# Performance work log

Hardware: AMD Instinct MI355X
Metric: run time of the kernel (lower is better)

The kernel has to match this reference:

```python
import jax, jax.numpy as jnp
import numpy as np

HEADS = 8
DIM_HEAD = 32
SCALE = DIM_HEAD ** -0.5
EPS = 1e-12  # F.normalize eps


def _rmsnorm_ch(t, g):
    # F.normalize(t, dim=1) * g * sqrt(C)  (normalize_dim=1)
    c = t.shape[1]
    norm = jnp.sqrt(jnp.sum(t * t, axis=1, keepdims=True))
    return t / jnp.maximum(norm, EPS) * g[None, :, None, None] * (c ** 0.5)


def setup_inputs() -> dict:
    key = jax.random.key(0)
    ks = jax.random.split(key, 4)
    B, C, H, W = 16, 256, 64, 64
    hidden = HEADS * DIM_HEAD  # 256
    x = jax.random.normal(ks[0], (B, C, H, W), dtype=jnp.float32)
    g1 = jnp.ones((C,), dtype=jnp.float32)
    # conv 1x1 weights stored as [out_ch, in_ch]
    w_qkv = jax.random.normal(ks[1], (hidden * 3, C), dtype=jnp.float32) * (1.0 / np.sqrt(C))
    w_out = jax.random.normal(ks[2], (C, hidden), dtype=jnp.float32) * (1.0 / np.sqrt(hidden))
    b_out = jnp.zeros((C,), dtype=jnp.float32)
    g2 = jnp.ones((C,), dtype=jnp.float32)
    return {"x": x, "g1": g1, "w_qkv": w_qkv, "w_out": w_out, "b_out": b_out, "g2": g2}


def reference(x, g1, w_qkv, w_out, b_out, g2):
    b, c, h, w = x.shape
    n = h * w
    xn = _rmsnorm_ch(x, g1)
    # 1x1 conv (no bias) == channel matmul
    qkv = jnp.einsum('oc,bchw->bohw', w_qkv, xn)
    q, k, v = jnp.split(qkv, 3, axis=1)
    # b (h c) x y -> b h c (x y)
    q = q.reshape(b, HEADS, DIM_HEAD, n)
    k = k.reshape(b, HEADS, DIM_HEAD, n)
    v = v.reshape(b, HEADS, DIM_HEAD, n)
    q = jax.nn.softmax(q, axis=-2) * SCALE  # softmax over dim_head
    k = jax.nn.softmax(k, axis=-1)          # softmax over sequence
    context = jnp.einsum('bhdn,bhen->bhde', k, v)  # [b,h,d,e] small
    out = jnp.einsum('bhde,bhdn->bhen', context, q)
    out = out.reshape(b, HEADS * DIM_HEAD, h, w)
    out = jnp.einsum('oc,bchw->bohw', w_out, out) + b_out[None, :, None, None]
    return _rmsnorm_ch(out, g2) + x
```

## Files before the change

### kernel.cpp

```cpp
#include <hip/hip_runtime.h>
#include <math.h>


#define B_ 16
#define C_ 256
#define N_ 4096
#define SCALE_ 0.17677669529663687f
#define EPS_ 1e-12f

typedef __attribute__((ext_vector_type(8))) short bf16x8;
typedef __attribute__((ext_vector_type(4))) float f32x4;

__device__ __forceinline__ ushort f2bf(float f) {
    union { float f; uint u; } x; x.f = f;
    uint r = (x.u + 0x7FFFu + ((x.u >> 16) & 1u)) >> 16;
    return (ushort)r;
}
__device__ __forceinline__ float bf2f(ushort s) {
    union { uint u; float f; } x; x.u = ((uint)s) << 16;
    return x.f;
}

__global__ __launch_bounds__(256) void k_prep(const float* __restrict__ w_qkv,
                                              const float* __restrict__ g1,
                                              ushort* __restrict__ Wp) {
    int o = blockIdx.x, c = threadIdx.x;
    Wp[(size_t)o * 256 + c] = f2bf(w_qkv[(size_t)o * 256 + c] * g1[c]);
}

__global__ __launch_bounds__(256) void k_xconv(const float* __restrict__ x,
                                               ushort* __restrict__ xnbT) {
    __shared__ float ssp[4][64];
    __shared__ float rinv_s[64];
    __shared__ ushort T[64][268];
    int b = blockIdx.y, n0 = blockIdx.x * 64;
    const float* xb = x + (size_t)b * C_ * N_ + n0;
    int t = threadIdx.x;
    int nl = t & 63, cg = t >> 6;
    float ss = 0.f;
    #pragma unroll 8
    for (int i = 0; i < 64; ++i) {
        float v = xb[(size_t)(cg * 64 + i) * N_ + nl];
        ss += v * v;
    }
    ssp[cg][nl] = ss;
    __syncthreads();
    if (t < 64)
        rinv_s[t] = 16.f / fmaxf(sqrtf(ssp[0][t] + ssp[1][t] + ssp[2][t] + ssp[3][t]), EPS_);
    __syncthreads();
    float rv = rinv_s[nl];
    #pragma unroll 8
    for (int i = 0; i < 64; ++i) {
        int c = cg * 64 + i;
        T[nl][c] = f2bf(xb[(size_t)c * N_ + nl] * rv);
    }
    __syncthreads();
    int j = t >> 2, ch = t & 3;
    ushort* orow = xnbT + ((size_t)b * N_ + n0 + j) * 256 + ch * 64;
    #pragma unroll
    for (int i = 0; i < 8; ++i)
        *(uint2*)&orow[i * 8] = *(const uint2*)&T[j][ch * 64 + i * 8],
        *(uint2*)&orow[i * 8 + 4] = *(const uint2*)&T[j][ch * 64 + i * 8 + 4];
}

__global__ __launch_bounds__(256) void k_gemm(const ushort* __restrict__ Wp,
                                              const ushort* __restrict__ xnbT,
                                              ushort* __restrict__ kvOut) {
    __shared__ ushort Asub[128][40];
    __shared__ ushort Bsub[128][40];
    const int b = blockIdx.z;
    const int wrow0 = 256 + blockIdx.y * 128;
    const int col0 = blockIdx.x * 128;
    const int t = threadIdx.x;
    const int l = t & 63, w = t >> 6;
    const int wr = w >> 1, wc = w & 1, grp = l >> 4;
    const ushort* xb = xnbT + (size_t)b * N_ * 256;
    f32x4 acc[4][4] = {};

    for (int k0 = 0; k0 < 256; k0 += 32) {
        int r = t >> 1, ko = (t & 1) * 16;
        const uint4* sa = (const uint4*)(Wp + (size_t)(wrow0 + r) * 256 + k0 + ko);
        *(uint4*)&Asub[r][ko]     = sa[0];
        *(uint4*)&Asub[r][ko + 8] = sa[1];
        const uint4* sb = (const uint4*)(xb + (size_t)(col0 + r) * 256 + k0 + ko);
        *(uint4*)&Bsub[r][ko]     = sb[0];
        *(uint4*)&Bsub[r][ko + 8] = sb[1];
        __syncthreads();
        bf16x8 af[4], bfv[4];
        #pragma unroll
        for (int m = 0; m < 4; ++m)
            af[m] = *(const bf16x8*)&Asub[wr * 64 + m * 16 + (l & 15)][grp * 8];
        #pragma unroll
        for (int n = 0; n < 4; ++n)
            bfv[n] = *(const bf16x8*)&Bsub[wc * 64 + n * 16 + (l & 15)][grp * 8];
        #pragma unroll
        for (int m = 0; m < 4; ++m)
            #pragma unroll
            for (int n = 0; n < 4; ++n)
                acc[m][n] = __builtin_amdgcn_mfma_f32_16x16x32_bf16(af[m], bfv[n], acc[m][n], 0, 0, 0);
        __syncthreads();
    }

    ushort* kvb = kvOut + (size_t)b * 512 * N_;
    #pragma unroll
    for (int n = 0; n < 4; ++n) {
        int cg = col0 + wc * 64 + n * 16 + (l & 15);
        #pragma unroll
        for (int m = 0; m < 4; ++m) {
            int rbase = wrow0 - 256 + wr * 64 + m * 16 + grp * 4;
            #pragma unroll
            for (int r = 0; r < 4; ++r)
                kvb[(size_t)(rbase + r) * N_ + cg] = f2bf(acc[m][n][r]);
        }
    }
}

__global__ __launch_bounds__(256) void k_ctxpart(const ushort* __restrict__ kv,
                                                 float* __restrict__ ctxp,
                                                 float* __restrict__ sums_p) {
    __shared__ float red[4][32][33];
    __shared__ float redp[4][32];
    int bh = blockIdx.x, s = blockIdx.y;
    int b = bh >> 3, h = bh & 7;
    int t = threadIdx.x, l = t & 63, w = t >> 6;
    const ushort* kb = kv + (size_t)b * 512 * N_ + (size_t)(h * 32) * N_;
    const ushort* vb = kv + (size_t)b * 512 * N_ + (size_t)(256 + h * 32) * N_;
    const int n0base = s * 1024 + w * 256;
    const int row = l & 15, grp = l >> 4;
    f32x4 acc[2][2] = {};
    float psA = 0.f, psB = 0.f;

    for (int it = 0; it < 8; ++it) {
        int n0 = n0base + it * 32 + grp * 8;
        bf16x8 k0 = *(const bf16x8*)&kb[(size_t)row * N_ + n0];
        bf16x8 k1 = *(const bf16x8*)&kb[(size_t)(row + 16) * N_ + n0];
        bf16x8 v0 = *(const bf16x8*)&vb[(size_t)row * N_ + n0];
        bf16x8 v1 = *(const bf16x8*)&vb[(size_t)(row + 16) * N_ + n0];
        bf16x8 p0, p1;
        #pragma unroll
        for (int j = 0; j < 8; ++j) {
            ushort r0 = f2bf(__expf(bf2f((ushort)k0[j])));
            ushort r1 = f2bf(__expf(bf2f((ushort)k1[j])));
            p0[j] = (short)r0; p1[j] = (short)r1;
            psA += bf2f(r0); psB += bf2f(r1);
        }
        acc[0][0] = __builtin_amdgcn_mfma_f32_16x16x32_bf16(p0, v0, acc[0][0], 0, 0, 0);
        acc[0][1] = __builtin_amdgcn_mfma_f32_16x16x32_bf16(p0, v1, acc[0][1], 0, 0, 0);
        acc[1][0] = __builtin_amdgcn_mfma_f32_16x16x32_bf16(p1, v0, acc[1][0], 0, 0, 0);
        acc[1][1] = __builtin_amdgcn_mfma_f32_16x16x32_bf16(p1, v1, acc[1][1], 0, 0, 0);
    }

    psA += __shfl_xor(psA, 16); psA += __shfl_xor(psA, 32);
    psB += __shfl_xor(psB, 16); psB += __shfl_xor(psB, 32);
    #pragma unroll
    for (int mi = 0; mi < 2; ++mi)
        #pragma unroll
        for (int ni = 0; ni < 2; ++ni)
            #pragma unroll
            for (int r = 0; r < 4; ++r)
                red[w][mi * 16 + grp * 4 + r][ni * 16 + row] = acc[mi][ni][r];
    if (l < 16) { redp[w][l] = psA; redp[w][16 + l] = psB; }
    __syncthreads();

    size_t base = (size_t)(s * 128 + bh) * 32;
    #pragma unroll
    for (int i = t; i < 1024; i += 256) {
        int d = i >> 5, e = i & 31;
        ctxp[(base + d) * 32 + e] =
            red[0][d][e] + red[1][d][e] + red[2][d][e] + red[3][d][e];
    }
    if (t < 32)
        sums_p[base + t] = redp[0][t] + redp[1][t] + redp[2][t] + redp[3][t];
}

__global__ __launch_bounds__(256) void k_fold(const float* __restrict__ w_out,
                                              const float* __restrict__ ctxp,
                                              const float* __restrict__ sums_p,
                                              ushort* __restrict__ M) {
    __shared__ float cn[32][33];
    __shared__ float sinv[32];
    int bh = blockIdx.x;
    int b = bh >> 3, h = bh & 7;
    int t = threadIdx.x;
    if (t < 32) {
        float st = 0.f;
        #pragma unroll
        for (int s = 0; s < 4; ++s) st += sums_p[(size_t)(s * 128 + bh) * 32 + t];
        sinv[t] = SCALE_ / st;
    }
    #pragma unroll
    for (int i = t; i < 1024; i += 256) {
        int d = i >> 5, e = i & 31;
        float cv = 0.f;
        #pragma unroll
        for (int s = 0; s < 4; ++s)
            cv += ctxp[((size_t)(s * 128 + bh) * 32 + d) * 32 + e];
        cn[e][d] = cv;
    }
    __syncthreads();
    float wreg[32];
    const float* wr = w_out + (size_t)t * 256 + h * 32;
    #pragma unroll
    for (int e = 0; e < 32; e += 4) {
        float4 wv = *(const float4*)&wr[e];
        wreg[e] = wv.x; wreg[e + 1] = wv.y; wreg[e + 2] = wv.z; wreg[e + 3] = wv.w;
    }
    float acc[32] = {};
    #pragma unroll
    for (int e = 0; e < 32; ++e) {
        float we = wreg[e];
        #pragma unroll
        for (int d = 0; d < 32; ++d) acc[d] += we * cn[e][d];
    }
    ushort* Mrow = M + ((size_t)b * 256 + t) * 256 + h * 32;
    #pragma unroll
    for (int d = 0; d < 32; ++d) Mrow[d] = f2bf(acc[d] * sinv[d]);
}

__global__ __launch_bounds__(512) void k_qfinal(const ushort* __restrict__ Wp,
                                                const ushort* __restrict__ xnbT,
                                                const ushort* __restrict__ M,
                                                const float* __restrict__ b_out,
                                                const float* __restrict__ g2,
                                                const float* __restrict__ x,
                                                float* __restrict__ out) {
    __shared__ ushort Asub[256][40];
    __shared__ ushort Bsub[64][40];
    __shared__ ushort qlds[64 * 256];
    __shared__ float ss2[8][64];
    const int b = blockIdx.y, col0 = blockIdx.x * 64;
    const int t = threadIdx.x, l = t & 63, w = t >> 6;
    const int lr = l & 15, grp = l >> 4;
    const ushort* xb = xnbT + (size_t)b * N_ * 256;
    f32x4 acc[2][4] = {};

    for (int k0 = 0; k0 < 256; k0 += 32) {
        { int r = t >> 1, ko = (t & 1) * 16;
          const uint4* sa = (const uint4*)(Wp + (size_t)r * 256 + k0 + ko);
          *(uint4*)&Asub[r][ko]     = sa[0];
          *(uint4*)&Asub[r][ko + 8] = sa[1]; }
        if (t < 128) {
          int r = t >> 1, ko = (t & 1) * 16;
          const uint4* sb = (const uint4*)(xb + (size_t)(col0 + r) * 256 + k0 + ko);
          *(uint4*)&Bsub[r][ko]     = sb[0];
          *(uint4*)&Bsub[r][ko + 8] = sb[1]; }
        __syncthreads();
        bf16x8 af[2], bfv[4];
        #pragma unroll
        for (int m = 0; m < 2; ++m)
            af[m] = *(const bf16x8*)&Asub[w * 32 + m * 16 + lr][grp * 8];
        #pragma unroll
        for (int n = 0; n < 4; ++n)
            bfv[n] = *(const bf16x8*)&Bsub[n * 16 + lr][grp * 8];
        #pragma unroll
        for (int m = 0; m < 2; ++m)
            #pragma unroll
            for (int n = 0; n < 4; ++n)
                acc[m][n] = __builtin_amdgcn_mfma_f32_16x16x32_bf16(af[m], bfv[n], acc[m][n], 0, 0, 0);
        __syncthreads();
    }

    #pragma unroll
    for (int n = 0; n < 4; ++n) {
        float f[2][4];
        #pragma unroll
        for (int m = 0; m < 2; ++m)
            #pragma unroll
            for (int r = 0; r < 4; ++r) f[m][r] = acc[m][n][r];
        float mx = -1e30f;
        #pragma unroll
        for (int r = 0; r < 4; ++r) mx = fmaxf(mx, fmaxf(f[0][r], f[1][r]));
        mx = fmaxf(mx, __shfl_xor(mx, 16));
        mx = fmaxf(mx, __shfl_xor(mx, 32));
        float s = 0.f;
        #pragma unroll
        for (int r = 0; r < 4; ++r) {
            f[0][r] = __expf(f[0][r] - mx); s += f[0][r];
            f[1][r] = __expf(f[1][r] - mx); s += f[1][r];
        }
        s += __shfl_xor(s, 16); s += __shfl_xor(s, 32);
        float inv = 1.f / s;
        int cl = n * 16 + lr;
        #pragma unroll
        for (int m = 0; m < 2; ++m) {
            int d = w * 32 + m * 16 + grp * 4;
            uint2 pk;
            pk.x = (uint)f2bf(f[m][0] * inv) | ((uint)f2bf(f[m][1] * inv) << 16);
            pk.y = (uint)f2bf(f[m][2] * inv) | ((uint)f2bf(f[m][3] * inv) << 16);
            uint off = (uint)(cl * 512 + d * 2) ^ (uint)((cl & 7) << 4);
            *(uint2*)((char*)qlds + off) = pk;
        }
    }

    f32x4 acc2[2][4] = {};
    const ushort* Mb = M + (size_t)b * 256 * 256;
    for (int k0 = 0; k0 < 256; k0 += 32) {
        { int r = t >> 1, ko = (t & 1) * 16;
          const uint4* sa = (const uint4*)(Mb + (size_t)r * 256 + k0 + ko);
          *(uint4*)&Asub[r][ko]     = sa[0];
          *(uint4*)&Asub[r][ko + 8] = sa[1]; }
        __syncthreads();
        bf16x8 af[2], bq[4];
        #pragma unroll
        for (int m = 0; m < 2; ++m)
            af[m] = *(const bf16x8*)&Asub[w * 32 + m * 16 + lr][grp * 8];
        #pragma unroll
        for (int n = 0; n < 4; ++n) {
            int row = n * 16 + lr;
            uint off = (uint)(row * 512 + (k0 + grp * 8) * 2) ^ (uint)((row & 7) << 4);
            bq[n] = *(const bf16x8*)((const char*)qlds + off);
        }
        #pragma unroll
        for (int m = 0; m < 2; ++m)
            #pragma unroll
            for (int n = 0; n < 4; ++n)
                acc2[m][n] = __builtin_amdgcn_mfma_f32_16x16x32_bf16(af[m], bq[n], acc2[m][n], 0, 0, 0);
        __syncthreads();
    }

    #pragma unroll
    for (int n = 0; n < 4; ++n) {
        float local = 0.f;
        #pragma unroll
        for (int m = 0; m < 2; ++m) {
            int obase = w * 32 + m * 16 + grp * 4;
            #pragma unroll
            for (int r = 0; r < 4; ++r) {
                float f = acc2[m][n][r] + b_out[obase + r];
                acc2[m][n][r] = f;
                local += f * f;
            }
        }
        local += __shfl_xor(local, 16);
        local += __shfl_xor(local, 32);
        if (grp == 0) ss2[w][n * 16 + lr] = local;
    }
    __syncthreads();
    const float* xb2 = x + (size_t)b * C_ * N_;
    float* ob = out + (size_t)b * C_ * N_;
    #pragma unroll
    for (int n = 0; n < 4; ++n) {
        int cl = n * 16 + lr;
        int cg = col0 + cl;
        float tot = ss2[0][cl] + ss2[1][cl] + ss2[2][cl] + ss2[3][cl]
                  + ss2[4][cl] + ss2[5][cl] + ss2[6][cl] + ss2[7][cl];
        float rs = 16.f / fmaxf(sqrtf(tot), EPS_);
        #pragma unroll
        for (int m = 0; m < 2; ++m) {
            int obase = w * 32 + m * 16 + grp * 4;
            #pragma unroll
            for (int r = 0; r < 4; ++r) {
                int o = obase + r;
                ob[(size_t)o * N_ + cg] = acc2[m][n][r] * rs * g2[o] + xb2[(size_t)o * N_ + cg];
            }
        }
    }
}

extern "C" void kernel_launch(void* const* d_in, const int* in_sizes, int n_in,
                              void* d_out, int out_size, void* d_ws, size_t ws_size,
                              hipStream_t stream) {
    const float* x     = (const float*)d_in[0];
    const float* g1    = (const float*)d_in[1];
    const float* w_qkv = (const float*)d_in[2];
    const float* w_out = (const float*)d_in[3];
    const float* b_out = (const float*)d_in[4];
    const float* g2    = (const float*)d_in[5];
    float* out = (float*)d_out;
    char* ws = (char*)d_ws;

    ushort* Wp     = (ushort*)(ws + 0);
    float*  ctxp   = (float*)(ws + 393216);
    float*  sums_p = (float*)(ws + 2490368);
    ushort* Mm     = (ushort*)(ws + 2555904);
    ushort* xnbT   = (ushort*)(ws + 4653056);
    ushort* kv     = (ushort*)(ws + 38207488);

    k_prep<<<768, 256, 0, stream>>>(w_qkv, g1, Wp);
    k_xconv<<<dim3(64, 16), 256, 0, stream>>>(x, xnbT);
    k_gemm<<<dim3(32, 4, 16), 256, 0, stream>>>(Wp, xnbT, kv);
    k_ctxpart<<<dim3(128, 4), 256, 0, stream>>>(kv, ctxp, sums_p);
    k_fold<<<128, 256, 0, stream>>>(w_out, ctxp, sums_p, Mm);
    k_qfinal<<<dim3(64, 16), 512, 0, stream>>>(Wp, xnbT, Mm, b_out, g2, x, out);
}
```

Before: 152.3 us.

## Stage full activation tile in swizzled LDS once, stream weights from global

In both GEMM kernels, the whole 256-deep activation tile is loaded into LDS once, using an XOR-swizzled layout, before the K loop. The weight and M operands are now read directly from global memory into MFMA fragments rather than staged through padded LDS tiles. This removes two barriers per K step and the per-step LDS staging. In exchange, weights are fetched from global (likely L2-resident) with no sharing across waves, and each block uses more LDS, which may lower occupancy.

```diff
diff --git a/kernel.cpp b/kernel.cpp
--- a/kernel.cpp
+++ b/kernel.cpp
@@ -66,45 +66,48 @@
 __global__ __launch_bounds__(256) void k_gemm(const ushort* __restrict__ Wp,
                                               const ushort* __restrict__ xnbT,
                                               ushort* __restrict__ kvOut) {
-    __shared__ ushort Asub[128][40];
-    __shared__ ushort Bsub[128][40];
+    __shared__ ushort Bsub[128 * 256];
     const int b = blockIdx.z;
     const int wrow0 = 256 + blockIdx.y * 128;
     const int col0 = blockIdx.x * 128;
-    const int t = threadIdx.x;
-    const int l = t & 63, w = t >> 6;
-    const int wr = w >> 1, wc = w & 1, grp = l >> 4;
+    const int t = threadIdx.x, l = t & 63, w = t >> 6;
+    const int wr = w >> 1, wc = w & 1, lr = l & 15, grp = l >> 4;
     const ushort* xb = xnbT + (size_t)b * N_ * 256;
+
+    {
+        int row = t >> 1, seg = t & 1;
+        const uint4* src = (const uint4*)(xb + (size_t)(col0 + row) * 256 + seg * 128);
+        uint base = (uint)(row * 512 + seg * 256);
+        uint sw = (uint)((row & 7) << 4);
+        #pragma unroll
+        for (int i = 0; i < 16; ++i)
+            *(uint4*)((char*)Bsub + ((base + i * 16) ^ sw)) = src[i];
+    }
+    __syncthreads();
+
     f32x4 acc[4][4] = {};
-
     for (int k0 = 0; k0 < 256; k0 += 32) {
-        int r = t >> 1, ko = (t & 1) * 16;
-        const uint4* sa = (const uint4*)(Wp + (size_t)(wrow0 + r) * 256 + k0 + ko);
-        *(uint4*)&Asub[r][ko]     = sa[0];
-        *(uint4*)&Asub[r][ko + 8] = sa[1];
-        const uint4* sb = (const uint4*)(xb + (size_t)(col0 + r) * 256 + k0 + ko);
-        *(uint4*)&Bsub[r][ko]     = sb[0];
-        *(uint4*)&Bsub[r][ko + 8] = sb[1];
-        __syncthreads();
-        bf16x8 af[4], bfv[4];
+        bf16x8 af[4], bf[4];
         #pragma unroll
         for (int m = 0; m < 4; ++m)
-            af[m] = *(const bf16x8*)&Asub[wr * 64 + m * 16 + (l & 15)][grp * 8];
-        #pragma unroll
-        for (int n = 0; n < 4; ++n)
-            bfv[n] = *(const bf16x8*)&Bsub[wc * 64 + n * 16 + (l & 15)][grp * 8];
+            af[m] = *(const bf16x8*)(Wp + (size_t)(wrow0 + wr * 64 + m * 16 + lr) * 256 + k0 + grp * 8);
+        #pragma unroll
+        for (int n = 0; n < 4; ++n) {
+            int row = wc * 64 + n * 16 + lr;
+            uint off = (uint)(row * 512 + (k0 + grp * 8) * 2) ^ (uint)((row & 7) << 4);
+            bf[n] = *(const bf16x8*)((const char*)Bsub + off);
+        }
         #pragma unroll
         for (int m = 0; m < 4; ++m)
             #pragma unroll
             for (int n = 0; n < 4; ++n)
-                acc[m][n] = __builtin_amdgcn_mfma_f32_16x16x32_bf16(af[m], bfv[n], acc[m][n], 0, 0, 0);
-        __syncthreads();
+                acc[m][n] = __builtin_amdgcn_mfma_f32_16x16x32_bf16(af[m], bf[n], acc[m][n], 0, 0, 0);
     }
 
     ushort* kvb = kvOut + (size_t)b * 512 * N_;
     #pragma unroll
     for (int n = 0; n < 4; ++n) {
-        int cg = col0 + wc * 64 + n * 16 + (l & 15);
+        int cg = col0 + wc * 64 + n * 16 + lr;
         #pragma unroll
         for (int m = 0; m < 4; ++m) {
             int rbase = wrow0 - 256 + wr * 64 + m * 16 + grp * 4;
@@ -224,40 +227,42 @@
                                                 const float* __restrict__ g2,
                                                 const float* __restrict__ x,
                                                 float* __restrict__ out) {
-    __shared__ ushort Asub[256][40];
-    __shared__ ushort Bsub[64][40];
+    __shared__ ushort Bsub[64 * 256];
     __shared__ ushort qlds[64 * 256];
     __shared__ float ss2[8][64];
     const int b = blockIdx.y, col0 = blockIdx.x * 64;
     const int t = threadIdx.x, l = t & 63, w = t >> 6;
     const int lr = l & 15, grp = l >> 4;
     const ushort* xb = xnbT + (size_t)b * N_ * 256;
+
+    {
+        int row = t >> 3, seg = t & 7;
+        const uint4* src = (const uint4*)(xb + (size_t)(col0 + row) * 256 + seg * 32);
+        uint base = (uint)(row * 512 + seg * 64);
+        uint sw = (uint)((row & 7) << 4);
+        #pragma unroll
+        for (int i = 0; i < 4; ++i)
+            *(uint4*)((char*)Bsub + ((base + i * 16) ^ sw)) = src[i];
+    }
+    __syncthreads();
+
     f32x4 acc[2][4] = {};
-
     for (int k0 = 0; k0 < 256; k0 += 32) {
-        { int r = t >> 1, ko = (t & 1) * 16;
-          const uint4* sa = (const uint4*)(Wp + (size_t)r * 256 + k0 + ko);
-          *(uint4*)&Asub[r][ko]     = sa[0];
-          *(uint4*)&Asub[r][ko + 8] = sa[1]; }
-        if (t < 128) {
-          int r = t >> 1, ko = (t & 1) * 16;
-          const uint4* sb = (const uint4*)(xb + (size_t)(col0 + r) * 256 + k0 + ko);
-          *(uint4*)&Bsub[r][ko]     = sb[0];
-          *(uint4*)&Bsub[r][ko + 8] = sb[1]; }
-        __syncthreads();
-        bf16x8 af[2], bfv[4];
-        #pragma unroll
-        for (int m = 0; m < 2; ++m)
-            af[m] = *(const bf16x8*)&Asub[w * 32 + m * 16 + lr][grp * 8];
-        #pragma unroll
-        for (int n = 0; n < 4; ++n)
-            bfv[n] = *(const bf16x8*)&Bsub[n * 16 + lr][grp * 8];
+        bf16x8 af[2], bf[4];
+        #pragma unroll
+        for (int m = 0; m < 2; ++m)
+            af[m] = *(const bf16x8*)(Wp + (size_t)(w * 32 + m * 16 + lr) * 256 + k0 + grp * 8);
+        #pragma unroll
+        for (int n = 0; n < 4; ++n) {
+            int row = n * 16 + lr;
+            uint off = (uint)(row * 512 + (k0 + grp * 8) * 2) ^ (uint)((row & 7) << 4);
+            bf[n] = *(const bf16x8*)((const char*)Bsub + off);
+        }
         #pragma unroll
         for (int m = 0; m < 2; ++m)
             #pragma unroll
             for (int n = 0; n < 4; ++n)
-                acc[m][n] = __builtin_amdgcn_mfma_f32_16x16x32_bf16(af[m], bfv[n], acc[m][n], 0, 0, 0);
-        __syncthreads();
+                acc[m][n] = __builtin_amdgcn_mfma_f32_16x16x32_bf16(af[m], bf[n], acc[m][n], 0, 0, 0);
     }
 
     #pragma unroll
@@ -291,19 +296,15 @@
             *(uint2*)((char*)qlds + off) = pk;
         }
     }
+    __syncthreads();
 
     f32x4 acc2[2][4] = {};
     const ushort* Mb = M + (size_t)b * 256 * 256;
     for (int k0 = 0; k0 < 256; k0 += 32) {
-        { int r = t >> 1, ko = (t & 1) * 16;
-          const uint4* sa = (const uint4*)(Mb + (size_t)r * 256 + k0 + ko);
-          *(uint4*)&Asub[r][ko]     = sa[0];
-          *(uint4*)&Asub[r][ko + 8] = sa[1]; }
-        __syncthreads();
         bf16x8 af[2], bq[4];
         #pragma unroll
         for (int m = 0; m < 2; ++m)
-            af[m] = *(const bf16x8*)&Asub[w * 32 + m * 16 + lr][grp * 8];
+            af[m] = *(const bf16x8*)(Mb + (size_t)(w * 32 + m * 16 + lr) * 256 + k0 + grp * 8);
         #pragma unroll
         for (int n = 0; n < 4; ++n) {
             int row = n * 16 + lr;
@@ -315,7 +316,6 @@
             #pragma unroll
             for (int n = 0; n < 4; ++n)
                 acc2[m][n] = __builtin_amdgcn_mfma_f32_16x16x32_bf16(af[m], bq[n], acc2[m][n], 0, 0, 0);
-        __syncthreads();
     }
 
     #pragma unroll
```

New measurement: 169.0 us. 1.11x slower.

## Load weight fragments directly from global and stage x tile once in LDS

Applied to the files above, without the earlier changes.

The k_qfinal kernel no longer stages the Wp and M weight tiles through shared memory each k-step. Each wave now reads its MFMA A-fragments straight from global memory, relying on cache since every block reads the same weights. The 64x256 x tile is loaded once into a swizzled LDS buffer, which is then reused for the softmaxed q, removing the per-iteration barriers and cutting LDS use. The risk is higher global/L2 traffic and load latency exposed in the MFMA loop. A minimum-blocks hint is added to launch_bounds.

```diff
diff --git a/kernel.cpp b/kernel.cpp
--- a/kernel.cpp
+++ b/kernel.cpp
@@ -217,48 +217,50 @@
     for (int d = 0; d < 32; ++d) Mrow[d] = f2bf(acc[d] * sinv[d]);
 }
 
-__global__ __launch_bounds__(512) void k_qfinal(const ushort* __restrict__ Wp,
-                                                const ushort* __restrict__ xnbT,
-                                                const ushort* __restrict__ M,
-                                                const float* __restrict__ b_out,
-                                                const float* __restrict__ g2,
-                                                const float* __restrict__ x,
-                                                float* __restrict__ out) {
-    __shared__ ushort Asub[256][40];
-    __shared__ ushort Bsub[64][40];
-    __shared__ ushort qlds[64 * 256];
+__global__ __launch_bounds__(512, 8) void k_qfinal(const ushort* __restrict__ Wp,
+                                                   const ushort* __restrict__ xnbT,
+                                                   const ushort* __restrict__ M,
+                                                   const float* __restrict__ b_out,
+                                                   const float* __restrict__ g2,
+                                                   const float* __restrict__ x,
+                                                   float* __restrict__ out) {
+    __shared__ ushort BQ[64 * 256];
     __shared__ float ss2[8][64];
     const int b = blockIdx.y, col0 = blockIdx.x * 64;
     const int t = threadIdx.x, l = t & 63, w = t >> 6;
     const int lr = l & 15, grp = l >> 4;
     const ushort* xb = xnbT + (size_t)b * N_ * 256;
+
+    {
+        int row = t >> 3, seg = t & 7;
+        const uint4* src = (const uint4*)(xb + (size_t)(col0 + row) * 256 + seg * 32);
+        uint base = (uint)(row * 512 + seg * 64);
+        uint sw = (uint)((row & 7) << 4);
+        #pragma unroll
+        for (int i = 0; i < 4; ++i)
+            *(uint4*)((char*)BQ + ((base + i * 16) ^ sw)) = src[i];
+    }
+    __syncthreads();
+
     f32x4 acc[2][4] = {};
-
     for (int k0 = 0; k0 < 256; k0 += 32) {
-        { int r = t >> 1, ko = (t & 1) * 16;
-          const uint4* sa = (const uint4*)(Wp + (size_t)r * 256 + k0 + ko);
-          *(uint4*)&Asub[r][ko]     = sa[0];
-          *(uint4*)&Asub[r][ko + 8] = sa[1]; }
-        if (t < 128) {
-          int r = t >> 1, ko = (t & 1) * 16;
-          const uint4* sb = (const uint4*)(xb + (size_t)(col0 + r) * 256 + k0 + ko);
-          *(uint4*)&Bsub[r][ko]     = sb[0];
-          *(uint4*)&Bsub[r][ko + 8] = sb[1]; }
-        __syncthreads();
-        bf16x8 af[2], bfv[4];
-        #pragma unroll
-        for (int m = 0; m < 2; ++m)
-            af[m] = *(const bf16x8*)&Asub[w * 32 + m * 16 + lr][grp * 8];
-        #pragma unroll
-        for (int n = 0; n < 4; ++n)
-            bfv[n] = *(const bf16x8*)&Bsub[n * 16 + lr][grp * 8];
+        bf16x8 af[2], bf[4];
+        #pragma unroll
+        for (int m = 0; m < 2; ++m)
+            af[m] = *(const bf16x8*)(Wp + (size_t)(w * 32 + m * 16 + lr) * 256 + k0 + grp * 8);
+        #pragma unroll
+        for (int n = 0; n < 4; ++n) {
+            int row = n * 16 + lr;
+            uint off = (uint)(row * 512 + (k0 + grp * 8) * 2) ^ (uint)((row & 7) << 4);
+            bf[n] = *(const bf16x8*)((const char*)BQ + off);
+        }
         #pragma unroll
         for (int m = 0; m < 2; ++m)
             #pragma unroll
             for (int n = 0; n < 4; ++n)
-                acc[m][n] = __builtin_amdgcn_mfma_f32_16x16x32_bf16(af[m], bfv[n], acc[m][n], 0, 0, 0);
-        __syncthreads();
-    }
+                acc[m][n] = __builtin_amdgcn_mfma_f32_16x16x32_bf16(af[m], bf[n], acc[m][n], 0, 0, 0);
+    }
+    __syncthreads();
 
     #pragma unroll
     for (int n = 0; n < 4; ++n) {
@@ -288,34 +290,29 @@
             pk.x = (uint)f2bf(f[m][0] * inv) | ((uint)f2bf(f[m][1] * inv) << 16);
             pk.y = (uint)f2bf(f[m][2] * inv) | ((uint)f2bf(f[m][3] * inv) << 16);
             uint off = (uint)(cl * 512 + d * 2) ^ (uint)((cl & 7) << 4);
-            *(uint2*)((char*)qlds + off) = pk;
-        }
-    }
+            *(uint2*)((char*)BQ + off) = pk;
+        }
+    }
+    __syncthreads();
 
     f32x4 acc2[2][4] = {};
     const ushort* Mb = M + (size_t)b * 256 * 256;
     for (int k0 = 0; k0 < 256; k0 += 32) {
-        { int r = t >> 1, ko = (t & 1) * 16;
-          const uint4* sa = (const uint4*)(Mb + (size_t)r * 256 + k0 + ko);
-          *(uint4*)&Asub[r][ko]     = sa[0];
-          *(uint4*)&Asub[r][ko + 8] = sa[1]; }
-        __syncthreads();
         bf16x8 af[2], bq[4];
         #pragma unroll
         for (int m = 0; m < 2; ++m)
-            af[m] = *(const bf16x8*)&Asub[w * 32 + m * 16 + lr][grp * 8];
+            af[m] = *(const bf16x8*)(Mb + (size_t)(w * 32 + m * 16 + lr) * 256 + k0 + grp * 8);
         #pragma unroll
         for (int n = 0; n < 4; ++n) {
             int row = n * 16 + lr;
             uint off = (uint)(row * 512 + (k0 + grp * 8) * 2) ^ (uint)((row & 7) << 4);
-            bq[n] = *(const bf16x8*)((const char*)qlds + off);
+            bq[n] = *(const bf16x8*)((const char*)BQ + off);
         }
         #pragma unroll
         for (int m = 0; m < 2; ++m)
             #pragma unroll
             for (int n = 0; n < 4; ++n)
                 acc2[m][n] = __builtin_amdgcn_mfma_f32_16x16x32_bf16(af[m], bq[n], acc2[m][n], 0, 0, 0);
-        __syncthreads();
     }
 
     #pragma unroll
```

After: 233.5 us. 1.53x slower.
